# Kernel tuning notes

Hardware: AMD Instinct MI355X
Metric: run time of the kernel (lower is better)

The kernel has to match this reference:

```python
import jax, jax.numpy as jnp
import numpy as np


def setup_inputs() -> dict:
    key = jax.random.key(0)
    ks = jax.random.split(key, 7)
    B, F, D = 1024, 32, 64
    H = [128, 128, 128]
    x = jax.random.normal(ks[0], (B, F, D), dtype=jnp.float32)
    # Conv1d(k=1) weights: (out, in) where in = prev_field * F, Kaiming-ish scale
    W0 = jax.random.normal(ks[1], (H[0], F * F), dtype=jnp.float32) * 0.02
    b0 = jnp.zeros((H[0],), dtype=jnp.float32)
    W1 = jax.random.normal(ks[2], (H[1], H[0] * F), dtype=jnp.float32) * 0.02
    b1 = jnp.zeros((H[1],), dtype=jnp.float32)
    W2 = jax.random.normal(ks[3], (H[2], H[1] * F), dtype=jnp.float32) * 0.02
    b2 = jnp.zeros((H[2],), dtype=jnp.float32)
    return {"x": x, "W0": W0, "b0": b0, "W1": W1, "b1": b1, "W2": W2, "b2": b2}


def reference(x, W0, b0, W1, b1, W2, b2):
    # CIN: per layer, outer product of current hidden with base fields along
    # embed dim, then 1x1 conv (channel mix) + ReLU. We fuse the bhmd
    # intermediate directly into the contraction: W reshaped to (o, h, m)
    # matches torch's reshape(b, h*m, d) channel ordering (h major, m minor).
    F = x.shape[1]
    x0 = x  # (b, m=F, d)
    h = x
    res = []
    for W, b in ((W0, b0), (W1, b1), (W2, b2)):
        o = W.shape[0]
        Wr = W.reshape(o, h.shape[1], F)  # (o, h, m)
        z = jnp.einsum('bhd,bmd,ohm->bod', h, x0, Wr) + b[None, :, None]
        h = jax.nn.relu(z)
        res.append(h)
    out = jnp.concatenate(res, axis=1)  # (b, sum(H), d)
    return jnp.sum(out, axis=-1)  # (b, sum(H))
```

## Files before the change

kernel.cpp:

```cpp
#include <hip/hip_runtime.h>
#include <stdint.h>


typedef __attribute__((ext_vector_type(8))) _Float16 f16x8;
typedef __attribute__((ext_vector_type(2))) _Float16 f16x2;
typedef __attribute__((ext_vector_type(4))) float f32x4;
typedef __attribute__((ext_vector_type(4))) int i32x4;

union AB {
  i32x4 i;
  f16x8 h;
  uint32_t u[4];
};

static __device__ __forceinline__ uint32_t pkmul(uint32_t a, uint32_t b) {
  f16x2 r = __builtin_bit_cast(f16x2, a) * __builtin_bit_cast(f16x2, b);
  return __builtin_bit_cast(uint32_t, r);
}
static __device__ __forceinline__ uint32_t pkcvt(float a, float b) {
  return __builtin_bit_cast(uint32_t, __builtin_amdgcn_cvt_pkrtz(a, b));
}

#define HP 136

__global__ __launch_bounds__(512, 4) void cin_main(
    const float* __restrict__ x, const uint16_t* __restrict__ wp,
    const float* __restrict__ bias0, const float* __restrict__ bias1,
    const float* __restrict__ bias2, float* __restrict__ out) {
  __shared__ __align__(16) uint16_t hT[2][64][HP];

  const int tid = threadIdx.x;
  const int w = tid >> 6, lane = tid & 63;
  const int p = w >> 2;
  const int wg = w & 3;
  const int q = lane >> 4;
  const int i = lane & 15;
  const int bb = blockIdx.x * 2;

  for (int e = tid; e < 4096; e += 512) {
    int p2 = e >> 11, m = (e >> 6) & 31, d = e & 63;
    hT[p2][d][m] =
        __builtin_bit_cast(uint16_t, (_Float16)x[(size_t)(bb + p2) * 2048 + m * 64 + d]);
  }
  __syncthreads();

  AB xf[4];
#pragma unroll
  for (int t = 0; t < 4; ++t)
    xf[t].i = *(const i32x4*)&hT[p][t * 16 + i][q * 8];

  f32x4 acc[4][2];

#pragma unroll
  for (int L = 0; L < 3; ++L) {
    const int Kch = (L == 0) ? 32 : 128;
    const uint16_t* wl = (L == 0) ? wp : (L == 1) ? wp + 131072 : wp + 655360;
    const float* bias = (L == 0) ? bias0 : (L == 1) ? bias1 : bias2;

    const uint16_t* wptr0 = wl + (size_t)(2 * wg + 0) * Kch * 512 + lane * 8;
    const uint16_t* wptr1 = wl + (size_t)(2 * wg + 1) * Kch * 512 + lane * 8;

#pragma unroll
    for (int t = 0; t < 4; ++t)
#pragma unroll
      for (int g = 0; g < 2; ++g) acc[t][g] = (f32x4){0.f, 0.f, 0.f, 0.f};

    AB wbuf[2][2][2];
    uint32_t hvA[4], hvB[4];

    auto loadSlot = [&](int s, int c) {
      int cw = (c < Kch) ? c : 0;
#pragma unroll
      for (int cc = 0; cc < 2; ++cc) {
        wbuf[s][cc][0].i = *(const i32x4*)(wptr0 + (size_t)(cw + cc) * 512);
        wbuf[s][cc][1].i = *(const i32x4*)(wptr1 + (size_t)(cw + cc) * 512);
      }
    };
    auto loadHv = [&](uint32_t (&hv)[4], int c) {
      int cw = (c < Kch) ? c : 0;
#pragma unroll
      for (int t = 0; t < 4; ++t)
        hv[t] = *(const uint32_t*)&hT[p][t * 16 + i][cw];
    };
    auto computePair = [&](const AB (&wb)[2][2], const uint32_t (&hv)[4]) {
#pragma unroll
      for (int cc = 0; cc < 2; ++cc)
#pragma unroll
        for (int t = 0; t < 4; ++t) {
          uint32_t hd = __builtin_amdgcn_perm(hv[t], hv[t],
                                              cc ? 0x03020302u : 0x01000100u);
          AB bf;
#pragma unroll
          for (int k = 0; k < 4; ++k) bf.u[k] = pkmul(hd, xf[t].u[k]);
          acc[t][0] = __builtin_amdgcn_mfma_f32_16x16x32_f16(wb[cc][0].h, bf.h, acc[t][0], 0, 0, 0);
          acc[t][1] = __builtin_amdgcn_mfma_f32_16x16x32_f16(wb[cc][1].h, bf.h, acc[t][1], 0, 0, 0);
        }
    };

    loadSlot(0, 0);
    loadSlot(1, 2);
    loadHv(hvA, 0);

#pragma unroll 1
    for (int c0 = 0; c0 < Kch; c0 += 4) {
      loadHv(hvB, c0 + 2);
      computePair(wbuf[0], hvA);
      loadSlot(0, c0 + 4);
      __builtin_amdgcn_sched_barrier(0);
      loadHv(hvA, c0 + 4);
      computePair(wbuf[1], hvB);
      loadSlot(1, c0 + 6);
      __builtin_amdgcn_sched_barrier(0);
    }

    f32x4 bv[2];
    bv[0] = *(const f32x4*)(bias + (2 * wg + 0) * 16 + q * 4);
    bv[1] = *(const f32x4*)(bias + (2 * wg + 1) * 16 + q * 4);
#pragma unroll
    for (int t = 0; t < 4; ++t)
#pragma unroll
      for (int g = 0; g < 2; ++g)
#pragma unroll
        for (int r = 0; r < 4; ++r)
          acc[t][g][r] = fmaxf(acc[t][g][r] + bv[g][r], 0.f);

    if (L < 2) {
      __syncthreads();
#pragma unroll
      for (int t = 0; t < 4; ++t)
#pragma unroll
        for (int g = 0; g < 2; ++g) {
          uint2 pk;
          pk.x = pkcvt(acc[t][g][0], acc[t][g][1]);
          pk.y = pkcvt(acc[t][g][2], acc[t][g][3]);
          *(uint2*)&hT[p][t * 16 + i][(2 * wg + g) * 16 + q * 4] = pk;
        }
    }

#pragma unroll
    for (int g = 0; g < 2; ++g)
#pragma unroll
      for (int r = 0; r < 4; ++r) {
        float s = acc[0][g][r] + acc[1][g][r] + acc[2][g][r] + acc[3][g][r];
        s += __shfl_xor(s, 1);
        s += __shfl_xor(s, 2);
        s += __shfl_xor(s, 4);
        s += __shfl_xor(s, 8);
        if (i == 0)
          out[(size_t)(bb + p) * 384 + L * 128 + (2 * wg + g) * 16 + q * 4 + r] = s;
      }

    if (L < 2) __syncthreads();
  }
}

__global__ void pack_w_all(const float* __restrict__ W0, const float* __restrict__ W1,
                           const float* __restrict__ W2, uint16_t* __restrict__ Wp) {
  int blk = blockIdx.x;
  const float* W;
  uint16_t* dst;
  int kshift;
  if (blk < 64)       { W = W0; dst = Wp;          kshift = 5; }
  else if (blk < 320) { W = W1; dst = Wp + 131072; kshift = 7; blk -= 64; }
  else                { W = W2; dst = Wp + 655360; kshift = 7; blk -= 320; }
  int idx = blk * 256 + threadIdx.x;
  int Kq = 1 << (kshift + 2);
  int o = idx >> (kshift + 2);
  int kq = idx & (Kq - 1);
  int c = kq >> 2, q = kq & 3;
  int ot = o >> 4, ii = o & 15;
  const float* src = W + ((size_t)o << (kshift + 5)) + kq * 8;
  uint4 val;
  val.x = pkcvt(src[0], src[1]);
  val.y = pkcvt(src[2], src[3]);
  val.z = pkcvt(src[4], src[5]);
  val.w = pkcvt(src[6], src[7]);
  *(uint4*)(dst + ((((size_t)ot << kshift) + c) << 9) + (q << 7) + (ii << 3)) = val;
}

extern "C" void kernel_launch(void* const* d_in, const int* in_sizes, int n_in,
                              void* d_out, int out_size, void* d_ws, size_t ws_size,
                              hipStream_t stream) {
  (void)in_sizes; (void)n_in; (void)out_size; (void)ws_size;
  const float* x  = (const float*)d_in[0];
  const float* W0 = (const float*)d_in[1];
  const float* b0 = (const float*)d_in[2];
  const float* W1 = (const float*)d_in[3];
  const float* b1 = (const float*)d_in[4];
  const float* W2 = (const float*)d_in[5];
  const float* b2 = (const float*)d_in[6];
  uint16_t* wpacked = (uint16_t*)d_ws;

  hipLaunchKernelGGL(pack_w_all, dim3(576), dim3(256), 0, stream, W0, W1, W2, wpacked);
  hipLaunchKernelGGL(cin_main, dim3(512), dim3(512), 0, stream,
                     x, wpacked, b0, b1, b2, (float*)d_out);
}
```

Before: 201.1 us.

## Retile CIN waves to split d across wave pairs and widen output groups

```diff
diff --git a/kernel.cpp b/kernel.cpp
--- a/kernel.cpp
+++ b/kernel.cpp
@@ -7,18 +7,15 @@
 typedef __attribute__((ext_vector_type(4))) float f32x4;
 typedef __attribute__((ext_vector_type(4))) int i32x4;
 
-union AB {
-  i32x4 i;
-  f16x8 h;
-  uint32_t u[4];
-};
-
 static __device__ __forceinline__ uint32_t pkmul(uint32_t a, uint32_t b) {
   f16x2 r = __builtin_bit_cast(f16x2, a) * __builtin_bit_cast(f16x2, b);
   return __builtin_bit_cast(uint32_t, r);
 }
 static __device__ __forceinline__ uint32_t pkcvt(float a, float b) {
   return __builtin_bit_cast(uint32_t, __builtin_amdgcn_cvt_pkrtz(a, b));
+}
+static __device__ __forceinline__ f16x8 asf16(i32x4 v) {
+  return __builtin_bit_cast(f16x8, v);
 }
 
 #define HP 136
@@ -28,11 +25,13 @@
     const float* __restrict__ bias0, const float* __restrict__ bias1,
     const float* __restrict__ bias2, float* __restrict__ out) {
   __shared__ __align__(16) uint16_t hT[2][64][HP];
+  __shared__ float sOut[2][2][128];
 
   const int tid = threadIdx.x;
   const int w = tid >> 6, lane = tid & 63;
-  const int p = w >> 2;
-  const int wg = w & 3;
+  const int p  = __builtin_amdgcn_readfirstlane(w >> 2);
+  const int th = __builtin_amdgcn_readfirstlane((w >> 1) & 1);
+  const int og = __builtin_amdgcn_readfirstlane(w & 1);
   const int q = lane >> 4;
   const int i = lane & 15;
   const int bb = blockIdx.x * 2;
@@ -44,12 +43,13 @@
   }
   __syncthreads();
 
-  AB xf[4];
-#pragma unroll
-  for (int t = 0; t < 4; ++t)
-    xf[t].i = *(const i32x4*)&hT[p][t * 16 + i][q * 8];
-
-  f32x4 acc[4][2];
+  i32x4 xf[2];
+#pragma unroll
+  for (int t2 = 0; t2 < 2; ++t2)
+    xf[t2] = *(const i32x4*)&hT[p][(2 * th + t2) * 16 + i][q * 8];
+
+  f32x4 acc[2][4];
+  const int loff = lane * 8;
 
 #pragma unroll
   for (int L = 0; L < 3; ++L) {
@@ -57,100 +57,122 @@
     const uint16_t* wl = (L == 0) ? wp : (L == 1) ? wp + 131072 : wp + 655360;
     const float* bias = (L == 0) ? bias0 : (L == 1) ? bias1 : bias2;
 
-    const uint16_t* wptr0 = wl + (size_t)(2 * wg + 0) * Kch * 512 + lane * 8;
-    const uint16_t* wptr1 = wl + (size_t)(2 * wg + 1) * Kch * 512 + lane * 8;
-
-#pragma unroll
-    for (int t = 0; t < 4; ++t)
-#pragma unroll
-      for (int g = 0; g < 2; ++g) acc[t][g] = (f32x4){0.f, 0.f, 0.f, 0.f};
-
-    AB wbuf[2][2][2];
-    uint32_t hvA[4], hvB[4];
-
-    auto loadSlot = [&](int s, int c) {
-      int cw = (c < Kch) ? c : 0;
+    const uint16_t* wb0 = wl + (size_t)(4 * og + 0) * Kch * 512;
+    const uint16_t* wb1 = wl + (size_t)(4 * og + 1) * Kch * 512;
+    const uint16_t* wb2 = wl + (size_t)(4 * og + 2) * Kch * 512;
+    const uint16_t* wb3 = wl + (size_t)(4 * og + 3) * Kch * 512;
+
+#pragma unroll
+    for (int t2 = 0; t2 < 2; ++t2)
+#pragma unroll
+      for (int g = 0; g < 4; ++g) acc[t2][g] = (f32x4){0.f, 0.f, 0.f, 0.f};
+
+    i32x4 wbuf[2][2][4];
+    uint2 hvA[2], hvB[2];
+    const uint16_t* hrow0 = &hT[p][(2 * th + 0) * 16 + i][0];
+    const uint16_t* hrow1 = &hT[p][(2 * th + 1) * 16 + i][0];
+
+    auto loadSlot = [&](int s, int co) {
 #pragma unroll
       for (int cc = 0; cc < 2; ++cc) {
-        wbuf[s][cc][0].i = *(const i32x4*)(wptr0 + (size_t)(cw + cc) * 512);
-        wbuf[s][cc][1].i = *(const i32x4*)(wptr1 + (size_t)(cw + cc) * 512);
+        wbuf[s][cc][0] = *(const i32x4*)(wb0 + co + cc * 512 + loff);
+        wbuf[s][cc][1] = *(const i32x4*)(wb1 + co + cc * 512 + loff);
+        wbuf[s][cc][2] = *(const i32x4*)(wb2 + co + cc * 512 + loff);
+        wbuf[s][cc][3] = *(const i32x4*)(wb3 + co + cc * 512 + loff);
       }
     };
-    auto loadHv = [&](uint32_t (&hv)[4], int c) {
-      int cw = (c < Kch) ? c : 0;
-#pragma unroll
-      for (int t = 0; t < 4; ++t)
-        hv[t] = *(const uint32_t*)&hT[p][t * 16 + i][cw];
+    auto loadHv = [&](uint2 (&hv)[2]) {
+      hv[0] = *(const uint2*)hrow0; hrow0 += 4;
+      hv[1] = *(const uint2*)hrow1; hrow1 += 4;
     };
-    auto computePair = [&](const AB (&wb)[2][2], const uint32_t (&hv)[4]) {
-#pragma unroll
-      for (int cc = 0; cc < 2; ++cc)
-#pragma unroll
-        for (int t = 0; t < 4; ++t) {
-          uint32_t hd = __builtin_amdgcn_perm(hv[t], hv[t],
-                                              cc ? 0x03020302u : 0x01000100u);
-          AB bf;
-#pragma unroll
-          for (int k = 0; k < 4; ++k) bf.u[k] = pkmul(hd, xf[t].u[k]);
-          acc[t][0] = __builtin_amdgcn_mfma_f32_16x16x32_f16(wb[cc][0].h, bf.h, acc[t][0], 0, 0, 0);
-          acc[t][1] = __builtin_amdgcn_mfma_f32_16x16x32_f16(wb[cc][1].h, bf.h, acc[t][1], 0, 0, 0);
+    auto computePair = [&](int s, uint32_t w0, uint32_t w1) {
+#pragma unroll
+      for (int cc = 0; cc < 2; ++cc) {
+        const uint32_t sel = cc ? 0x03020302u : 0x01000100u;
+#pragma unroll
+        for (int t2 = 0; t2 < 2; ++t2) {
+          uint32_t word = t2 ? w1 : w0;
+          uint32_t hd = __builtin_amdgcn_perm(word, word, sel);
+          i32x4 bf;
+#pragma unroll
+          for (int k = 0; k < 4; ++k) bf[k] = (int)pkmul(hd, (uint32_t)xf[t2][k]);
+#pragma unroll
+          for (int g = 0; g < 4; ++g)
+            acc[t2][g] = __builtin_amdgcn_mfma_f32_16x16x32_f16(
+                asf16(wbuf[s][cc][g]), asf16(bf), acc[t2][g], 0, 0, 0);
         }
+      }
     };
 
     loadSlot(0, 0);
-    loadSlot(1, 2);
-    loadHv(hvA, 0);
+    loadSlot(1, 1024);
+    int co = 2048;
+    const int comax = (Kch - 4) * 512;
+    loadHv(hvA);
+    __builtin_amdgcn_sched_barrier(0);
 
 #pragma unroll 1
-    for (int c0 = 0; c0 < Kch; c0 += 4) {
-      loadHv(hvB, c0 + 2);
-      computePair(wbuf[0], hvA);
-      loadSlot(0, c0 + 4);
-      __builtin_amdgcn_sched_barrier(0);
-      loadHv(hvA, c0 + 4);
-      computePair(wbuf[1], hvB);
-      loadSlot(1, c0 + 6);
-      __builtin_amdgcn_sched_barrier(0);
-    }
-
-    f32x4 bv[2];
-    bv[0] = *(const f32x4*)(bias + (2 * wg + 0) * 16 + q * 4);
-    bv[1] = *(const f32x4*)(bias + (2 * wg + 1) * 16 + q * 4);
-#pragma unroll
-    for (int t = 0; t < 4; ++t)
-#pragma unroll
-      for (int g = 0; g < 2; ++g)
+    for (int c0 = 0; c0 < Kch; c0 += 8) {
+      loadHv(hvB);
+      computePair(0, hvA[0].x, hvA[1].x);
+      loadSlot(0, co);
+      __builtin_amdgcn_sched_barrier(0);
+      computePair(1, hvA[0].y, hvA[1].y);
+      loadSlot(1, co + 1024);
+      __builtin_amdgcn_sched_barrier(0);
+      co = (co + 2048 < comax) ? co + 2048 : comax;
+      loadHv(hvA);
+      computePair(0, hvB[0].x, hvB[1].x);
+      loadSlot(0, co);
+      __builtin_amdgcn_sched_barrier(0);
+      computePair(1, hvB[0].y, hvB[1].y);
+      loadSlot(1, co + 1024);
+      __builtin_amdgcn_sched_barrier(0);
+      co = (co + 2048 < comax) ? co + 2048 : comax;
+    }
+
+#pragma unroll
+    for (int g = 0; g < 4; ++g) {
+      f32x4 bv = *(const f32x4*)(bias + (4 * og + g) * 16 + q * 4);
+#pragma unroll
+      for (int t2 = 0; t2 < 2; ++t2)
 #pragma unroll
         for (int r = 0; r < 4; ++r)
-          acc[t][g][r] = fmaxf(acc[t][g][r] + bv[g][r], 0.f);
+          acc[t2][g][r] = fmaxf(acc[t2][g][r] + bv[r], 0.f);
+    }
+
+    __syncthreads();
 
     if (L < 2) {
-      __syncthreads();
-#pragma unroll
-      for (int t = 0; t < 4; ++t)
-#pragma unroll
-        for (int g = 0; g < 2; ++g) {
+#pragma unroll
+      for (int t2 = 0; t2 < 2; ++t2)
+#pragma unroll
+        for (int g = 0; g < 4; ++g) {
           uint2 pk;
-          pk.x = pkcvt(acc[t][g][0], acc[t][g][1]);
-          pk.y = pkcvt(acc[t][g][2], acc[t][g][3]);
-          *(uint2*)&hT[p][t * 16 + i][(2 * wg + g) * 16 + q * 4] = pk;
+          pk.x = pkcvt(acc[t2][g][0], acc[t2][g][1]);
+          pk.y = pkcvt(acc[t2][g][2], acc[t2][g][3]);
+          *(uint2*)&hT[p][(2 * th + t2) * 16 + i][(4 * og + g) * 16 + q * 4] = pk;
         }
     }
 
 #pragma unroll
-    for (int g = 0; g < 2; ++g)
+    for (int g = 0; g < 4; ++g)
 #pragma unroll
       for (int r = 0; r < 4; ++r) {
-        float s = acc[0][g][r] + acc[1][g][r] + acc[2][g][r] + acc[3][g][r];
+        float s = acc[0][g][r] + acc[1][g][r];
         s += __shfl_xor(s, 1);
         s += __shfl_xor(s, 2);
         s += __shfl_xor(s, 4);
         s += __shfl_xor(s, 8);
-        if (i == 0)
-          out[(size_t)(bb + p) * 384 + L * 128 + (2 * wg + g) * 16 + q * 4 + r] = s;
+        if (i == 0) sOut[p][th][(4 * og + g) * 16 + q * 4 + r] = s;
       }
 
-    if (L < 2) __syncthreads();
+    __syncthreads();
+
+    if (tid < 256) {
+      int b2 = tid >> 7, o = tid & 127;
+      out[(size_t)(bb + b2) * 384 + L * 128 + o] = sOut[b2][0][o] + sOut[b2][1][o];
+    }
   }
 }
 
```

Measured after the change: 370.4 us. 84.2% more time.
